# Optimization experiments

Hardware: AMD Instinct MI355X
Metric: run time of the kernel (lower is better)

The kernel has to match this reference:

```python
import jax, jax.numpy as jnp
import numpy as np

DIM = 4096
M = 64  # m = sqrt(dim)
B = 16384


def setup_inputs() -> dict:
    key = jax.random.key(0)
    kx, kl, kr = jax.random.split(key, 3)
    x = jax.random.normal(kx, (B, DIM), dtype=jnp.float32)
    # Module initializes L, R as identity blocks; perturb slightly so the
    # transform is non-trivial while staying faithful to the parameter shapes.
    eye = jnp.broadcast_to(jnp.eye(M, dtype=jnp.float32), (M, M, M))
    L = eye + 0.02 * jax.random.normal(kl, (M, M, M), dtype=jnp.float32)
    R = eye + 0.02 * jax.random.normal(kr, (M, M, M), dtype=jnp.float32)
    bias = jnp.zeros((DIM,), dtype=jnp.float32)
    return {"x": x, "L": L, "R": R, "bias": bias}


def reference(x, L, R, bias):
    # y = P L P^T R x  (Monarch, Dao 2022 Def 3.1) + bias
    Bn = x.shape[0]
    h = x.reshape(Bn, M, M)                 # (B, m, m)
    h = jnp.einsum('bki,kij->bkj', h, R)    # block-diagonal R
    h = jnp.swapaxes(h, 1, 2)               # P^T (stride permutation)
    h = jnp.einsum('bki,kij->bkj', h, L)    # block-diagonal L
    h = jnp.swapaxes(h, 1, 2)               # P (transpose back)
    return h.reshape(Bn, DIM) + bias
```

## Files before the change

### kernel.cpp

```cpp
#include <hip/hip_runtime.h>
#include <stdint.h>


typedef __attribute__((ext_vector_type(8))) short short8;
typedef __attribute__((ext_vector_type(4))) float f32x4;

#define LDS_SB 36
#define LDS_SJ (16 * LDS_SB + 4)
#define LDS_WORDS (64 * LDS_SJ)
#define LDS_BYTES (LDS_WORDS * 4)

__device__ __forceinline__ unsigned short f2bf(float f) {
    unsigned int u = __float_as_uint(f);
    u += 0x7FFFu + ((u >> 16) & 1u);
    return (unsigned short)(u >> 16);
}
__device__ __forceinline__ float bf2f(unsigned short h) {
    return __uint_as_float(((unsigned int)h) << 16);
}
__device__ __forceinline__ f32x4 zero4() {
    f32x4 z; z[0] = 0.f; z[1] = 0.f; z[2] = 0.f; z[3] = 0.f; return z;
}
__device__ __forceinline__ void split2x4(f32x4 a, f32x4 b, short8& hi, short8& lo) {
#pragma unroll
    for (int e = 0; e < 4; ++e) {
        unsigned short h = f2bf(a[e]);
        hi[e] = (short)h; lo[e] = (short)f2bf(a[e] - bf2f(h));
        unsigned short h2 = f2bf(b[e]);
        hi[e + 4] = (short)h2; lo[e + 4] = (short)f2bf(b[e] - bf2f(h2));
    }
}

__global__ void monarch_prep(const float* __restrict__ L, const float* __restrict__ R,
                             unsigned short* __restrict__ Rt_hi, unsigned short* __restrict__ Rt_lo,
                             unsigned short* __restrict__ Lt_hi, unsigned short* __restrict__ Lt_lo)
{
    int t = blockIdx.x * blockDim.x + threadIdx.x;
    bool isL = t >= 262144;
    int u = t & 262143;
    int blk = u >> 12;
    int row = (u >> 6) & 63;
    int col = u & 63;
    const float* src = isL ? L : R;
    float v = src[u];
    int c    = row >> 5;
    int hq   = (row >> 3) & 3;
    int e    = row & 7;
    int lane = hq * 16 + (col & 15);
    int tile = col >> 4;
    int idx  = (((blk * 2 + c) * 4 + tile) * 64 + lane) * 8 + e;
    unsigned short h  = f2bf(v);
    unsigned short lo = f2bf(v - bf2f(h));
    if (isL) { Lt_hi[idx] = h; Lt_lo[idx] = lo; }
    else     { Rt_hi[idx] = h; Rt_lo[idx] = lo; }
}

template<bool USE_WS>
__global__ __launch_bounds__(1024, 4) void monarch_fused(
    const float* __restrict__ x,
    const float* __restrict__ L,
    const float* __restrict__ R,
    const float* __restrict__ bias,
    const unsigned short* __restrict__ Rt_hi,
    const unsigned short* __restrict__ Rt_lo,
    const unsigned short* __restrict__ Lt_hi,
    const unsigned short* __restrict__ Lt_lo,
    float* __restrict__ out)
{
    extern __shared__ float h1[];
    const int tid  = threadIdx.x;
    const int wid  = tid >> 6;
    const int lane = tid & 63;
    const int lr   = lane & 15;
    const int lq   = lane >> 4;
    const long b0  = (long)blockIdx.x * 16;

    f32x4 acc[4][4];
#pragma unroll
    for (int a = 0; a < 4; ++a)
#pragma unroll
        for (int b = 0; b < 4; ++b) acc[a][b] = zero4();

    const float* xrow = x + (b0 + lr) * 4096;

#pragma unroll
    for (int g = 0; g < 2; ++g) {
#pragma unroll
        for (int kk = 0; kk < 2; ++kk) {
            const int k  = g * 32 + wid * 2 + kk;
            const int kl = wid * 2 + kk;
            const float* p = xrow + k * 64 + lq * 8;
            f32x4 xa0 = *(const f32x4*)(p);
            f32x4 xa1 = *(const f32x4*)(p + 4);
            f32x4 xb0 = *(const f32x4*)(p + 32);
            f32x4 xb1 = *(const f32x4*)(p + 36);
            f32x4 cf[4];
#pragma unroll
            for (int jt = 0; jt < 4; ++jt) cf[jt] = zero4();
#pragma unroll
            for (int c = 0; c < 2; ++c) {
                short8 ah, al;
                if (c == 0) split2x4(xa0, xa1, ah, al);
                else        split2x4(xb0, xb1, ah, al);
#pragma unroll
                for (int jt = 0; jt < 4; ++jt) {
                    short8 bh, bl;
                    if (USE_WS) {
                        const int idx = (((k * 2 + c) * 4 + jt) * 64 + lane) * 8;
                        bh = *(const short8*)(Rt_hi + idx);
                        bl = *(const short8*)(Rt_lo + idx);
                    } else {
                        float rv0[4], rv1[4];
#pragma unroll
                        for (int e = 0; e < 4; ++e) {
                            rv0[e] = R[k * 4096 + (c * 32 + lq * 8 + e) * 64 + jt * 16 + lr];
                            rv1[e] = R[k * 4096 + (c * 32 + lq * 8 + 4 + e) * 64 + jt * 16 + lr];
                        }
                        f32x4 r0 = *(const f32x4*)rv0, r1 = *(const f32x4*)rv1;
                        split2x4(r0, r1, bh, bl);
                    }
                    cf[jt] = __builtin_amdgcn_mfma_f32_16x16x32_bf16(ah, bh, cf[jt], 0, 0, 0);
                    cf[jt] = __builtin_amdgcn_mfma_f32_16x16x32_bf16(al, bh, cf[jt], 0, 0, 0);
                    cf[jt] = __builtin_amdgcn_mfma_f32_16x16x32_bf16(ah, bl, cf[jt], 0, 0, 0);
                }
            }
#pragma unroll
            for (int jt = 0; jt < 4; ++jt) {
                const int j = jt * 16 + lr;
#pragma unroll
                for (int r = 0; r < 4; ++r) {
                    const int b = lq * 4 + r;
                    h1[j * LDS_SJ + b * LDS_SB + kl] = cf[jt][r];
                }
            }
        }
        __syncthreads();
#pragma unroll
        for (int jj = 0; jj < 4; ++jj) {
            const int j = wid * 4 + jj;
            const float* hp = &h1[j * LDS_SJ + lr * LDS_SB + lq * 8];
            f32x4 h0 = *(const f32x4*)(hp);
            f32x4 h4 = *(const f32x4*)(hp + 4);
            short8 ah, al;
            split2x4(h0, h4, ah, al);
#pragma unroll
            for (int lt = 0; lt < 4; ++lt) {
                short8 bh, bl;
                if (USE_WS) {
                    const int idx = (((j * 2 + g) * 4 + lt) * 64 + lane) * 8;
                    bh = *(const short8*)(Lt_hi + idx);
                    bl = *(const short8*)(Lt_lo + idx);
                } else {
                    float lv0[4], lv1[4];
#pragma unroll
                    for (int e = 0; e < 4; ++e) {
                        lv0[e] = L[j * 4096 + (g * 32 + lq * 8 + e) * 64 + lt * 16 + lr];
                        lv1[e] = L[j * 4096 + (g * 32 + lq * 8 + 4 + e) * 64 + lt * 16 + lr];
                    }
                    f32x4 l0 = *(const f32x4*)lv0, l1 = *(const f32x4*)lv1;
                    split2x4(l0, l1, bh, bl);
                }
                acc[jj][lt] = __builtin_amdgcn_mfma_f32_16x16x32_bf16(ah, bh, acc[jj][lt], 0, 0, 0);
                acc[jj][lt] = __builtin_amdgcn_mfma_f32_16x16x32_bf16(al, bh, acc[jj][lt], 0, 0, 0);
                acc[jj][lt] = __builtin_amdgcn_mfma_f32_16x16x32_bf16(ah, bl, acc[jj][lt], 0, 0, 0);
            }
        }
        __syncthreads();
    }

    const f32x4 bv = *(const f32x4*)(bias + tid * 4);
#pragma unroll
    for (int p = 0; p < 2; ++p) {
        if ((lq >> 1) == p) {
#pragma unroll
            for (int jj = 0; jj < 4; ++jj) {
                const int j = wid * 4 + jj;
#pragma unroll
                for (int lt = 0; lt < 4; ++lt) {
                    const int l = lt * 16 + lr;
#pragma unroll
                    for (int r = 0; r < 4; ++r) {
                        const int b7 = (lq & 1) * 4 + r;
                        const int w = b7 * 4096 + l * 64 + j;
                        const int unit = w >> 2;
                        const int phys = (unit ^ ((unit >> 4) & 15)) * 4 + (w & 3);
                        h1[phys] = acc[jj][lt][r];
                    }
                }
            }
        }
        __syncthreads();
#pragma unroll
        for (int it = 0; it < 8; ++it) {
            const int u = it * 1024 + tid;
            const int phys = u ^ ((u >> 4) & 15);
            f32x4 v = *(const f32x4*)(&h1[phys * 4]);
            v[0] += bv[0]; v[1] += bv[1]; v[2] += bv[2]; v[3] += bv[3];
            *(f32x4*)(&out[(b0 + p * 8 + it) * 4096 + tid * 4]) = v;
        }
        if (p == 0) __syncthreads();
    }
}

extern "C" void kernel_launch(void* const* d_in, const int* in_sizes, int n_in,
                              void* d_out, int out_size, void* d_ws, size_t ws_size,
                              hipStream_t stream)
{
    const float* x    = (const float*)d_in[0];
    const float* L    = (const float*)d_in[1];
    const float* R    = (const float*)d_in[2];
    const float* bias = (const float*)d_in[3];
    float* out = (float*)d_out;

    const size_t WS_NEED = 4ull * 262144ull * sizeof(unsigned short);
    const bool use_ws = (d_ws != nullptr) && (ws_size >= WS_NEED);

    if (use_ws) {
        unsigned short* rt_hi = (unsigned short*)d_ws;
        unsigned short* rt_lo = rt_hi + 262144;
        unsigned short* lt_hi = rt_lo + 262144;
        unsigned short* lt_lo = lt_hi + 262144;
        monarch_prep<<<2048, 256, 0, stream>>>(L, R, rt_hi, rt_lo, lt_hi, lt_lo);
        (void)hipFuncSetAttribute(reinterpret_cast<const void*>(&monarch_fused<true>),
                                  hipFuncAttributeMaxDynamicSharedMemorySize, LDS_BYTES);
        monarch_fused<true><<<1024, 1024, LDS_BYTES, stream>>>(
            x, L, R, bias, rt_hi, rt_lo, lt_hi, lt_lo, out);
    } else {
        (void)hipFuncSetAttribute(reinterpret_cast<const void*>(&monarch_fused<false>),
                                  hipFuncAttributeMaxDynamicSharedMemorySize, LDS_BYTES);
        monarch_fused<false><<<1024, 1024, LDS_BYTES, stream>>>(
            x, L, R, bias, nullptr, nullptr, nullptr, nullptr, out);
    }
}
```

Measured before the change: 567.5 us.

## Make fused Monarch kernel persistent with 512 threads and prefetched x rows

Launches 256 persistent workgroups of 512 threads (8 waves), each looping over four 16-row batch chunks instead of one chunk per 1024-thread block. Each wave handles 4 k-blocks and 8 j-blocks, and prefetches the next x slice into registers so global loads overlap the MFMA work. Output staging now uses vectorized f32x4 LDS writes. The cost is a larger register footprint (acc doubles to 8x4) and fewer waves per CU, so latency hiding depends on the prefetch.

```diff
diff --git a/kernel.cpp b/kernel.cpp
--- a/kernel.cpp
+++ b/kernel.cpp
@@ -56,7 +56,7 @@
 }
 
 template<bool USE_WS>
-__global__ __launch_bounds__(1024, 4) void monarch_fused(
+__global__ __launch_bounds__(512, 2) void monarch_fused(
     const float* __restrict__ x,
     const float* __restrict__ L,
     const float* __restrict__ R,
@@ -73,132 +73,174 @@
     const int lane = tid & 63;
     const int lr   = lane & 15;
     const int lq   = lane >> 4;
-    const long b0  = (long)blockIdx.x * 16;
-
-    f32x4 acc[4][4];
-#pragma unroll
-    for (int a = 0; a < 4; ++a)
-#pragma unroll
-        for (int b = 0; b < 4; ++b) acc[a][b] = zero4();
-
-    const float* xrow = x + (b0 + lr) * 4096;
-
-#pragma unroll
-    for (int g = 0; g < 2; ++g) {
-#pragma unroll
-        for (int kk = 0; kk < 2; ++kk) {
-            const int k  = g * 32 + wid * 2 + kk;
-            const int kl = wid * 2 + kk;
-            const float* p = xrow + k * 64 + lq * 8;
-            f32x4 xa0 = *(const f32x4*)(p);
-            f32x4 xa1 = *(const f32x4*)(p + 4);
-            f32x4 xb0 = *(const f32x4*)(p + 32);
-            f32x4 xb1 = *(const f32x4*)(p + 36);
-            f32x4 cf[4];
-#pragma unroll
-            for (int jt = 0; jt < 4; ++jt) cf[jt] = zero4();
-#pragma unroll
-            for (int c = 0; c < 2; ++c) {
+    const int wg   = blockIdx.x;
+
+    const f32x4 bv0 = *(const f32x4*)(bias + tid * 4);
+    const f32x4 bv1 = *(const f32x4*)(bias + tid * 4 + 2048);
+
+    f32x4 xpre[4];
+    {
+        const float* pn = x + ((long)(wg * 16 + lr)) * 4096 + (wid * 4) * 64 + lq * 8;
+        xpre[0] = *(const f32x4*)(pn);
+        xpre[1] = *(const f32x4*)(pn + 4);
+        xpre[2] = *(const f32x4*)(pn + 32);
+        xpre[3] = *(const f32x4*)(pn + 36);
+    }
+
+    for (int c = 0; c < 4; ++c) {
+        const long bchunk = (long)(c * 256 + wg) * 16;
+        const float* xr = x + (bchunk + lr) * 4096;
+
+        f32x4 acc[8][4];
+#pragma unroll
+        for (int a = 0; a < 8; ++a)
+#pragma unroll
+            for (int b = 0; b < 4; ++b) acc[a][b] = zero4();
+
+#pragma unroll
+        for (int g = 0; g < 2; ++g) {
+#pragma unroll
+            for (int kk = 0; kk < 4; ++kk) {
+                const int k  = g * 32 + wid * 4 + kk;
+                const int kl = wid * 4 + kk;
+                f32x4 x0, x1, x2, x3;
+                if (kk == 0) {
+                    x0 = xpre[0]; x1 = xpre[1]; x2 = xpre[2]; x3 = xpre[3];
+                } else {
+                    const float* p = xr + k * 64 + lq * 8;
+                    x0 = *(const f32x4*)(p);
+                    x1 = *(const f32x4*)(p + 4);
+                    x2 = *(const f32x4*)(p + 32);
+                    x3 = *(const f32x4*)(p + 36);
+                }
+                if (kk == 3) {
+                    const float* pn;
+                    if (g == 0) {
+                        pn = xr + (32 + wid * 4) * 64 + lq * 8;
+                    } else {
+                        const int nc = (c + 1) & 3;
+                        pn = x + ((long)((nc * 256 + wg) * 16 + lr)) * 4096 + (wid * 4) * 64 + lq * 8;
+                    }
+                    xpre[0] = *(const f32x4*)(pn);
+                    xpre[1] = *(const f32x4*)(pn + 4);
+                    xpre[2] = *(const f32x4*)(pn + 32);
+                    xpre[3] = *(const f32x4*)(pn + 36);
+                }
+                short8 ah0, al0, ah1, al1;
+                split2x4(x0, x1, ah0, al0);
+                split2x4(x2, x3, ah1, al1);
+                f32x4 cf[4];
+#pragma unroll
+                for (int jt = 0; jt < 4; ++jt) cf[jt] = zero4();
+#pragma unroll
+                for (int c2 = 0; c2 < 2; ++c2) {
+                    const short8 ah = c2 ? ah1 : ah0;
+                    const short8 al = c2 ? al1 : al0;
+#pragma unroll
+                    for (int jt = 0; jt < 4; ++jt) {
+                        short8 bh, bl;
+                        if (USE_WS) {
+                            const int idx = (((k * 2 + c2) * 4 + jt) * 64 + lane) * 8;
+                            bh = *(const short8*)(Rt_hi + idx);
+                            bl = *(const short8*)(Rt_lo + idx);
+                        } else {
+                            float rv0[4], rv1[4];
+#pragma unroll
+                            for (int e = 0; e < 4; ++e) {
+                                rv0[e] = R[k * 4096 + (c2 * 32 + lq * 8 + e) * 64 + jt * 16 + lr];
+                                rv1[e] = R[k * 4096 + (c2 * 32 + lq * 8 + 4 + e) * 64 + jt * 16 + lr];
+                            }
+                            f32x4 r0 = *(const f32x4*)rv0, r1 = *(const f32x4*)rv1;
+                            split2x4(r0, r1, bh, bl);
+                        }
+                        cf[jt] = __builtin_amdgcn_mfma_f32_16x16x32_bf16(ah, bh, cf[jt], 0, 0, 0);
+                        cf[jt] = __builtin_amdgcn_mfma_f32_16x16x32_bf16(al, bh, cf[jt], 0, 0, 0);
+                        cf[jt] = __builtin_amdgcn_mfma_f32_16x16x32_bf16(ah, bl, cf[jt], 0, 0, 0);
+                    }
+                }
+#pragma unroll
+                for (int jt = 0; jt < 4; ++jt) {
+                    const int j = jt * 16 + lr;
+#pragma unroll
+                    for (int r = 0; r < 4; ++r) {
+                        const int b = lq * 4 + r;
+                        h1[j * LDS_SJ + b * LDS_SB + kl] = cf[jt][r];
+                    }
+                }
+            }
+            __syncthreads();
+#pragma unroll
+            for (int jj = 0; jj < 8; ++jj) {
+                const int j = wid * 8 + jj;
+                const float* hp = &h1[j * LDS_SJ + lr * LDS_SB + lq * 8];
+                f32x4 h0 = *(const f32x4*)(hp);
+                f32x4 h4 = *(const f32x4*)(hp + 4);
                 short8 ah, al;
-                if (c == 0) split2x4(xa0, xa1, ah, al);
-                else        split2x4(xb0, xb1, ah, al);
-#pragma unroll
-                for (int jt = 0; jt < 4; ++jt) {
+                split2x4(h0, h4, ah, al);
+#pragma unroll
+                for (int lt = 0; lt < 4; ++lt) {
                     short8 bh, bl;
                     if (USE_WS) {
-                        const int idx = (((k * 2 + c) * 4 + jt) * 64 + lane) * 8;
-                        bh = *(const short8*)(Rt_hi + idx);
-                        bl = *(const short8*)(Rt_lo + idx);
+                        const int idx = (((j * 2 + g) * 4 + lt) * 64 + lane) * 8;
+                        bh = *(const short8*)(Lt_hi + idx);
+                        bl = *(const short8*)(Lt_lo + idx);
                     } else {
-                        float rv0[4], rv1[4];
+                        float lv0[4], lv1[4];
 #pragma unroll
                         for (int e = 0; e < 4; ++e) {
-                            rv0[e] = R[k * 4096 + (c * 32 + lq * 8 + e) * 64 + jt * 16 + lr];
-                            rv1[e] = R[k * 4096 + (c * 32 + lq * 8 + 4 + e) * 64 + jt * 16 + lr];
+                            lv0[e] = L[j * 4096 + (g * 32 + lq * 8 + e) * 64 + lt * 16 + lr];
+                            lv1[e] = L[j * 4096 + (g * 32 + lq * 8 + 4 + e) * 64 + lt * 16 + lr];
                         }
-                        f32x4 r0 = *(const f32x4*)rv0, r1 = *(const f32x4*)rv1;
-                        split2x4(r0, r1, bh, bl);
-                    }
-                    cf[jt] = __builtin_amdgcn_mfma_f32_16x16x32_bf16(ah, bh, cf[jt], 0, 0, 0);
-                    cf[jt] = __builtin_amdgcn_mfma_f32_16x16x32_bf16(al, bh, cf[jt], 0, 0, 0);
-                    cf[jt] = __builtin_amdgcn_mfma_f32_16x16x32_bf16(ah, bl, cf[jt], 0, 0, 0);
-                }
-            }
-#pragma unroll
-            for (int jt = 0; jt < 4; ++jt) {
-                const int j = jt * 16 + lr;
-#pragma unroll
-                for (int r = 0; r < 4; ++r) {
-                    const int b = lq * 4 + r;
-                    h1[j * LDS_SJ + b * LDS_SB + kl] = cf[jt][r];
-                }
-            }
+                        f32x4 l0 = *(const f32x4*)lv0, l1 = *(const f32x4*)lv1;
+                        split2x4(l0, l1, bh, bl);
+                    }
+                    acc[jj][lt] = __builtin_amdgcn_mfma_f32_16x16x32_bf16(ah, bh, acc[jj][lt], 0, 0, 0);
+                    acc[jj][lt] = __builtin_amdgcn_mfma_f32_16x16x32_bf16(al, bh, acc[jj][lt], 0, 0, 0);
+                    acc[jj][lt] = __builtin_amdgcn_mfma_f32_16x16x32_bf16(ah, bl, acc[jj][lt], 0, 0, 0);
+                }
+            }
+            __syncthreads();
         }
-        __syncthreads();
-#pragma unroll
-        for (int jj = 0; jj < 4; ++jj) {
-            const int j = wid * 4 + jj;
-            const float* hp = &h1[j * LDS_SJ + lr * LDS_SB + lq * 8];
-            f32x4 h0 = *(const f32x4*)(hp);
-            f32x4 h4 = *(const f32x4*)(hp + 4);
-            short8 ah, al;
-            split2x4(h0, h4, ah, al);
-#pragma unroll
-            for (int lt = 0; lt < 4; ++lt) {
-                short8 bh, bl;
-                if (USE_WS) {
-                    const int idx = (((j * 2 + g) * 4 + lt) * 64 + lane) * 8;
-                    bh = *(const short8*)(Lt_hi + idx);
-                    bl = *(const short8*)(Lt_lo + idx);
-                } else {
-                    float lv0[4], lv1[4];
-#pragma unroll
-                    for (int e = 0; e < 4; ++e) {
-                        lv0[e] = L[j * 4096 + (g * 32 + lq * 8 + e) * 64 + lt * 16 + lr];
-                        lv1[e] = L[j * 4096 + (g * 32 + lq * 8 + 4 + e) * 64 + lt * 16 + lr];
-                    }
-                    f32x4 l0 = *(const f32x4*)lv0, l1 = *(const f32x4*)lv1;
-                    split2x4(l0, l1, bh, bl);
-                }
-                acc[jj][lt] = __builtin_amdgcn_mfma_f32_16x16x32_bf16(ah, bh, acc[jj][lt], 0, 0, 0);
-                acc[jj][lt] = __builtin_amdgcn_mfma_f32_16x16x32_bf16(al, bh, acc[jj][lt], 0, 0, 0);
-                acc[jj][lt] = __builtin_amdgcn_mfma_f32_16x16x32_bf16(ah, bl, acc[jj][lt], 0, 0, 0);
-            }
-        }
-        __syncthreads();
-    }
-
-    const f32x4 bv = *(const f32x4*)(bias + tid * 4);
-#pragma unroll
-    for (int p = 0; p < 2; ++p) {
-        if ((lq >> 1) == p) {
-#pragma unroll
-            for (int jj = 0; jj < 4; ++jj) {
-                const int j = wid * 4 + jj;
+
+#pragma unroll
+        for (int p2 = 0; p2 < 2; ++p2) {
+            if ((lq >> 1) == p2) {
 #pragma unroll
                 for (int lt = 0; lt < 4; ++lt) {
                     const int l = lt * 16 + lr;
 #pragma unroll
                     for (int r = 0; r < 4; ++r) {
                         const int b7 = (lq & 1) * 4 + r;
-                        const int w = b7 * 4096 + l * 64 + j;
-                        const int unit = w >> 2;
-                        const int phys = (unit ^ ((unit >> 4) & 15)) * 4 + (w & 3);
-                        h1[phys] = acc[jj][lt][r];
-                    }
-                }
-            }
+#pragma unroll
+                        for (int q = 0; q < 2; ++q) {
+                            const int w = b7 * 4096 + l * 64 + wid * 8 + q * 4;
+                            const int unit = w >> 2;
+                            const int phys = unit ^ ((unit >> 4) & 15);
+                            f32x4 v;
+                            v[0] = acc[q * 4 + 0][lt][r];
+                            v[1] = acc[q * 4 + 1][lt][r];
+                            v[2] = acc[q * 4 + 2][lt][r];
+                            v[3] = acc[q * 4 + 3][lt][r];
+                            *(f32x4*)(&h1[phys * 4]) = v;
+                        }
+                    }
+                }
+            }
+            __syncthreads();
+#pragma unroll
+            for (int row = 0; row < 8; ++row) {
+#pragma unroll
+                for (int hf = 0; hf < 2; ++hf) {
+                    const int u = row * 1024 + hf * 512 + tid;
+                    const int phys = u ^ ((u >> 4) & 15);
+                    f32x4 v = *(const f32x4*)(&h1[phys * 4]);
+                    const f32x4 bv = hf ? bv1 : bv0;
+                    v[0] += bv[0]; v[1] += bv[1]; v[2] += bv[2]; v[3] += bv[3];
+                    *(f32x4*)(&out[(bchunk + p2 * 8 + row) * 4096 + hf * 2048 + tid * 4]) = v;
+                }
+            }
+            __syncthreads();
         }
-        __syncthreads();
-#pragma unroll
-        for (int it = 0; it < 8; ++it) {
-            const int u = it * 1024 + tid;
-            const int phys = u ^ ((u >> 4) & 15);
-            f32x4 v = *(const f32x4*)(&h1[phys * 4]);
-            v[0] += bv[0]; v[1] += bv[1]; v[2] += bv[2]; v[3] += bv[3];
-            *(f32x4*)(&out[(b0 + p * 8 + it) * 4096 + tid * 4]) = v;
-        }
-        if (p == 0) __syncthreads();
     }
 }
 
@@ -223,12 +265,12 @@
         monarch_prep<<<2048, 256, 0, stream>>>(L, R, rt_hi, rt_lo, lt_hi, lt_lo);
         (void)hipFuncSetAttribute(reinterpret_cast<const void*>(&monarch_fused<true>),
                                   hipFuncAttributeMaxDynamicSharedMemorySize, LDS_BYTES);
-        monarch_fused<true><<<1024, 1024, LDS_BYTES, stream>>>(
+        monarch_fused<true><<<256, 512, LDS_BYTES, stream>>>(
             x, L, R, bias, rt_hi, rt_lo, lt_hi, lt_lo, out);
     } else {
         (void)hipFuncSetAttribute(reinterpret_cast<const void*>(&monarch_fused<false>),
                                   hipFuncAttributeMaxDynamicSharedMemorySize, LDS_BYTES);
-        monarch_fused<false><<<1024, 1024, LDS_BYTES, stream>>>(
+        monarch_fused<false><<<256, 512, LDS_BYTES, stream>>>(
             x, L, R, bias, nullptr, nullptr, nullptr, nullptr, out);
     }
 }
```

Result: slower. 1.343 ms (+136.7%).

## Software-pipeline Monarch stages with double-buffered LDS and prefetched x loads

Applied to the files above, without the earlier changes.

Splits the two-stage block-diagonal matmul into four 16-block chunks processed in a software pipeline. The next chunk's x loads are issued and its stage-1 MFMAs run while stage 2 consumes the previous chunk from a double-buffered LDS tile. LDS writes become f32x4 stores with a rotating slot swizzle, and the epilogue packs four outputs per vector store. This adds LDS footprint and lowers launch bounds occupancy from 4 to 3, trading occupancy for overlap. Stage 2 now feeds K=32 MFMAs with half the lanes zeroed, which doubles the stage-2 MFMA count.

```diff
diff --git a/kernel.cpp b/kernel.cpp
--- a/kernel.cpp
+++ b/kernel.cpp
@@ -5,9 +5,9 @@
 typedef __attribute__((ext_vector_type(8))) short short8;
 typedef __attribute__((ext_vector_type(4))) float f32x4;
 
-#define LDS_SB 36
-#define LDS_SJ (16 * LDS_SB + 4)
-#define LDS_WORDS (64 * LDS_SJ)
+#define SJ_U 260
+#define UBUF (64 * SJ_U)
+#define LDS_WORDS (2 * UBUF)
 #define LDS_BYTES (LDS_WORDS * 4)
 
 __device__ __forceinline__ unsigned short f2bf(float f) {
@@ -56,7 +56,7 @@
 }
 
 template<bool USE_WS>
-__global__ __launch_bounds__(1024, 4) void monarch_fused(
+__global__ __launch_bounds__(1024, 3) void monarch_fused(
     const float* __restrict__ x,
     const float* __restrict__ L,
     const float* __restrict__ R,
@@ -73,6 +73,7 @@
     const int lane = tid & 63;
     const int lr   = lane & 15;
     const int lq   = lane >> 4;
+    const int lq1  = lq & 1;
     const long b0  = (long)blockIdx.x * 16;
 
     f32x4 acc[4][4];
@@ -82,124 +83,165 @@
         for (int b = 0; b < 4; ++b) acc[a][b] = zero4();
 
     const float* xrow = x + (b0 + lr) * 4096;
-
-#pragma unroll
-    for (int g = 0; g < 2; ++g) {
-#pragma unroll
-        for (int kk = 0; kk < 2; ++kk) {
-            const int k  = g * 32 + wid * 2 + kk;
-            const int kl = wid * 2 + kk;
-            const float* p = xrow + k * 64 + lq * 8;
-            f32x4 xa0 = *(const f32x4*)(p);
-            f32x4 xa1 = *(const f32x4*)(p + 4);
-            f32x4 xb0 = *(const f32x4*)(p + 32);
-            f32x4 xb1 = *(const f32x4*)(p + 36);
-            f32x4 cf[4];
-#pragma unroll
-            for (int jt = 0; jt < 4; ++jt) cf[jt] = zero4();
-#pragma unroll
-            for (int c = 0; c < 2; ++c) {
-                short8 ah, al;
-                if (c == 0) split2x4(xa0, xa1, ah, al);
-                else        split2x4(xb0, xb1, ah, al);
-#pragma unroll
-                for (int jt = 0; jt < 4; ++jt) {
-                    short8 bh, bl;
-                    if (USE_WS) {
-                        const int idx = (((k * 2 + c) * 4 + jt) * 64 + lane) * 8;
-                        bh = *(const short8*)(Rt_hi + idx);
-                        bl = *(const short8*)(Rt_lo + idx);
-                    } else {
-                        float rv0[4], rv1[4];
-#pragma unroll
-                        for (int e = 0; e < 4; ++e) {
-                            rv0[e] = R[k * 4096 + (c * 32 + lq * 8 + e) * 64 + jt * 16 + lr];
-                            rv1[e] = R[k * 4096 + (c * 32 + lq * 8 + 4 + e) * 64 + jt * 16 + lr];
-                        }
-                        f32x4 r0 = *(const f32x4*)rv0, r1 = *(const f32x4*)rv1;
-                        split2x4(r0, r1, bh, bl);
-                    }
-                    cf[jt] = __builtin_amdgcn_mfma_f32_16x16x32_bf16(ah, bh, cf[jt], 0, 0, 0);
-                    cf[jt] = __builtin_amdgcn_mfma_f32_16x16x32_bf16(al, bh, cf[jt], 0, 0, 0);
-                    cf[jt] = __builtin_amdgcn_mfma_f32_16x16x32_bf16(ah, bl, cf[jt], 0, 0, 0);
+    const int jbase = wid * 4;
+
+    f32x4 xr[4];
+
+#define X_ISSUE(U)                                                        \
+    {                                                                     \
+        const float* p = xrow + (((U) * 16 + wid) << 6) + lq * 8;         \
+        xr[0] = *(const f32x4*)(p);                                       \
+        xr[1] = *(const f32x4*)(p + 4);                                   \
+        xr[2] = *(const f32x4*)(p + 32);                                  \
+        xr[3] = *(const f32x4*)(p + 36);                                  \
+    }
+
+#define S1_COMPUTE(U)                                                     \
+    {                                                                     \
+        const int kg   = (U) * 16 + wid;                                  \
+        const int boff = ((U) & 1) * UBUF;                                \
+        short8 ah0, al0, ah1, al1;                                        \
+        split2x4(xr[0], xr[1], ah0, al0);                                 \
+        split2x4(xr[2], xr[3], ah1, al1);                                 \
+        f32x4 cf[4];                                                      \
+        _Pragma("unroll")                                                 \
+        for (int jt = 0; jt < 4; ++jt) cf[jt] = zero4();                  \
+        _Pragma("unroll")                                                 \
+        for (int c2 = 0; c2 < 2; ++c2) {                                  \
+            const short8 ah = c2 ? ah1 : ah0;                             \
+            const short8 al = c2 ? al1 : al0;                             \
+            _Pragma("unroll")                                             \
+            for (int jt = 0; jt < 4; ++jt) {                              \
+                short8 bh, bl;                                            \
+                if (USE_WS) {                                             \
+                    const int idx = (((kg * 2 + c2) * 4 + jt) * 64 + lane) * 8; \
+                    bh = *(const short8*)(Rt_hi + idx);                   \
+                    bl = *(const short8*)(Rt_lo + idx);                   \
+                } else {                                                  \
+                    float rv0[4], rv1[4];                                 \
+                    _Pragma("unroll")                                     \
+                    for (int e = 0; e < 4; ++e) {                         \
+                        rv0[e] = R[kg * 4096 + (c2 * 32 + lq * 8 + e) * 64 + jt * 16 + lr]; \
+                        rv1[e] = R[kg * 4096 + (c2 * 32 + lq * 8 + 4 + e) * 64 + jt * 16 + lr]; \
+                    }                                                     \
+                    f32x4 r0 = *(const f32x4*)rv0, r1 = *(const f32x4*)rv1; \
+                    split2x4(r0, r1, bh, bl);                             \
+                }                                                         \
+                cf[jt] = __builtin_amdgcn_mfma_f32_16x16x32_bf16(ah, bh, cf[jt], 0, 0, 0); \
+                cf[jt] = __builtin_amdgcn_mfma_f32_16x16x32_bf16(al, bh, cf[jt], 0, 0, 0); \
+                cf[jt] = __builtin_amdgcn_mfma_f32_16x16x32_bf16(ah, bl, cf[jt], 0, 0, 0); \
+            }                                                             \
+        }                                                                 \
+        const int s = (lq + (wid >> 2)) & 3;                              \
+        _Pragma("unroll")                                                 \
+        for (int jt = 0; jt < 4; ++jt) {                                  \
+            const int j = jt * 16 + lr;                                   \
+            *(f32x4*)(&h1[boff + j * SJ_U + wid * 16 + 4 * s]) = cf[jt];  \
+        }                                                                 \
+    }
+
+#define S2_CONSUME(U)                                                     \
+    {                                                                     \
+        const int boff = ((U) & 1) * UBUF;                                \
+        const int s_lo = ((lr >> 2) + 2 * lq1) & 3;                       \
+        const int s_hi = (s_lo + 1) & 3;                                  \
+        _Pragma("unroll")                                                 \
+        for (int jj = 0; jj < 4; ++jj) {                                  \
+            const int j = jbase + jj;                                     \
+            const float* hb = &h1[boff + j * SJ_U + lq1 * 128 + (lr & 3)]; \
+            float ha[8];                                                  \
+            _Pragma("unroll")                                             \
+            for (int e = 0; e < 4; ++e) {                                 \
+                ha[e]     = (lq < 2) ? hb[e * 16 + 4 * s_lo]      : 0.0f; \
+                ha[4 + e] = (lq < 2) ? hb[64 + e * 16 + 4 * s_hi] : 0.0f; \
+            }                                                             \
+            f32x4 h0, h4;                                                 \
+            _Pragma("unroll")                                             \
+            for (int e = 0; e < 4; ++e) { h0[e] = ha[e]; h4[e] = ha[4 + e]; } \
+            short8 ah, al;                                                \
+            split2x4(h0, h4, ah, al);                                     \
+            const int lane2 = (2 * ((U) & 1) + lq1) * 16 + lr;            \
+            _Pragma("unroll")                                             \
+            for (int lt = 0; lt < 4; ++lt) {                              \
+                short8 bh, bl;                                            \
+                if (USE_WS) {                                             \
+                    const int idx = (((j * 2 + ((U) >> 1)) * 4 + lt) * 64 + lane2) * 8; \
+                    bh = *(const short8*)(Lt_hi + idx);                   \
+                    bl = *(const short8*)(Lt_lo + idx);                   \
+                } else {                                                  \
+                    float lv0[4], lv1[4];                                 \
+                    _Pragma("unroll")                                     \
+                    for (int e = 0; e < 4; ++e) {                         \
+                        lv0[e] = L[j * 4096 + ((U) * 16 + lq1 * 8 + e) * 64 + lt * 16 + lr]; \
+                        lv1[e] = L[j * 4096 + ((U) * 16 + lq1 * 8 + 4 + e) * 64 + lt * 16 + lr]; \
+                    }                                                     \
+                    f32x4 l0 = *(const f32x4*)lv0, l1 = *(const f32x4*)lv1; \
+                    split2x4(l0, l1, bh, bl);                             \
+                }                                                         \
+                acc[jj][lt] = __builtin_amdgcn_mfma_f32_16x16x32_bf16(ah, bh, acc[jj][lt], 0, 0, 0); \
+                acc[jj][lt] = __builtin_amdgcn_mfma_f32_16x16x32_bf16(al, bh, acc[jj][lt], 0, 0, 0); \
+                acc[jj][lt] = __builtin_amdgcn_mfma_f32_16x16x32_bf16(ah, bl, acc[jj][lt], 0, 0, 0); \
+            }                                                             \
+        }                                                                 \
+    }
+
+    X_ISSUE(0)
+    S1_COMPUTE(0)
+    __syncthreads();
+
+#pragma unroll
+    for (int u = 0; u < 4; ++u) {
+        if (u < 3) { X_ISSUE(u + 1) }
+        switch (u) {
+            case 0: S2_CONSUME(0) break;
+            case 1: S2_CONSUME(1) break;
+            case 2: S2_CONSUME(2) break;
+            default: S2_CONSUME(3) break;
+        }
+        if (u < 3) {
+            switch (u) {
+                case 0: S1_COMPUTE(1) break;
+                case 1: S1_COMPUTE(2) break;
+                default: S1_COMPUTE(3) break;
+            }
+        }
+        __syncthreads();
+    }
+
+    const f32x4 bv = *(const f32x4*)(bias + tid * 4);
+#pragma unroll
+    for (int p = 0; p < 2; ++p) {
+        if ((lq >> 1) == p) {
+#pragma unroll
+            for (int lt = 0; lt < 4; ++lt) {
+                const int l = lt * 16 + lr;
+#pragma unroll
+                for (int r = 0; r < 4; ++r) {
+                    const int b7 = lq1 * 4 + r;
+                    const int w = b7 * 4096 + l * 64 + jbase;
+                    const int unit = w >> 2;
+                    const int phys = unit ^ ((unit >> 4) & 15);
+                    f32x4 v;
+                    v[0] = acc[0][lt][r]; v[1] = acc[1][lt][r];
+                    v[2] = acc[2][lt][r]; v[3] = acc[3][lt][r];
+                    *(f32x4*)(&h1[phys * 4]) = v;
                 }
             }
-#pragma unroll
-            for (int jt = 0; jt < 4; ++jt) {
-                const int j = jt * 16 + lr;
-#pragma unroll
-                for (int r = 0; r < 4; ++r) {
-                    const int b = lq * 4 + r;
-                    h1[j * LDS_SJ + b * LDS_SB + kl] = cf[jt][r];
-                }
-            }
         }
         __syncthreads();
 #pragma unroll
-        for (int jj = 0; jj < 4; ++jj) {
-            const int j = wid * 4 + jj;
-            const float* hp = &h1[j * LDS_SJ + lr * LDS_SB + lq * 8];
-            f32x4 h0 = *(const f32x4*)(hp);
-            f32x4 h4 = *(const f32x4*)(hp + 4);
-            short8 ah, al;
-            split2x4(h0, h4, ah, al);
-#pragma unroll
-            for (int lt = 0; lt < 4; ++lt) {
-                short8 bh, bl;
-                if (USE_WS) {
-                    const int idx = (((j * 2 + g) * 4 + lt) * 64 + lane) * 8;
-                    bh = *(const short8*)(Lt_hi + idx);
-                    bl = *(const short8*)(Lt_lo + idx);
-                } else {
-                    float lv0[4], lv1[4];
-#pragma unroll
-                    for (int e = 0; e < 4; ++e) {
-                        lv0[e] = L[j * 4096 + (g * 32 + lq * 8 + e) * 64 + lt * 16 + lr];
-                        lv1[e] = L[j * 4096 + (g * 32 + lq * 8 + 4 + e) * 64 + lt * 16 + lr];
-                    }
-                    f32x4 l0 = *(const f32x4*)lv0, l1 = *(const f32x4*)lv1;
-                    split2x4(l0, l1, bh, bl);
-                }
-                acc[jj][lt] = __builtin_amdgcn_mfma_f32_16x16x32_bf16(ah, bh, acc[jj][lt], 0, 0, 0);
-                acc[jj][lt] = __builtin_amdgcn_mfma_f32_16x16x32_bf16(al, bh, acc[jj][lt], 0, 0, 0);
-                acc[jj][lt] = __builtin_amdgcn_mfma_f32_16x16x32_bf16(ah, bl, acc[jj][lt], 0, 0, 0);
-            }
-        }
-        __syncthreads();
-    }
-
-    const f32x4 bv = *(const f32x4*)(bias + tid * 4);
-#pragma unroll
-    for (int p = 0; p < 2; ++p) {
-        if ((lq >> 1) == p) {
-#pragma unroll
-            for (int jj = 0; jj < 4; ++jj) {
-                const int j = wid * 4 + jj;
-#pragma unroll
-                for (int lt = 0; lt < 4; ++lt) {
-                    const int l = lt * 16 + lr;
-#pragma unroll
-                    for (int r = 0; r < 4; ++r) {
-                        const int b7 = (lq & 1) * 4 + r;
-                        const int w = b7 * 4096 + l * 64 + j;
-                        const int unit = w >> 2;
-                        const int phys = (unit ^ ((unit >> 4) & 15)) * 4 + (w & 3);
-                        h1[phys] = acc[jj][lt][r];
-                    }
-                }
-            }
-        }
-        __syncthreads();
-#pragma unroll
         for (int it = 0; it < 8; ++it) {
-            const int u = it * 1024 + tid;
-            const int phys = u ^ ((u >> 4) & 15);
+            const int ui = it * 1024 + tid;
+            const int phys = ui ^ ((ui >> 4) & 15);
             f32x4 v = *(const f32x4*)(&h1[phys * 4]);
             v[0] += bv[0]; v[1] += bv[1]; v[2] += bv[2]; v[3] += bv[3];
             *(f32x4*)(&out[(b0 + p * 8 + it) * 4096 + tid * 4]) = v;
         }
         if (p == 0) __syncthreads();
     }
+#undef X_ISSUE
+#undef S1_COMPUTE
+#undef S2_CONSUME
 }
 
 extern "C" void kernel_launch(void* const* d_in, const int* in_sizes, int n_in,
```

Result: slower. 613.2 us (+8.1%).
